# Kernel optimization log

Measured on AMD Instinct MI355X. Metric: run time of the kernel, lower is better.

## Reference

```python
import jax, jax.numpy as jnp
import numpy as np

B, S, HID = 2, 2048, 1024
H, KV, D = 16, 8, 64
NDIM = 2          # position_ids.shape[-1]
EPS = 1e-6
SCALING = 1.0


def _rms_norm(x, w=None, eps=EPS):
    # matches _RMSNorm: fp32 compute, optional learnable scale
    xf = x.astype(jnp.float32)
    n = xf * jax.lax.rsqrt(jnp.mean(xf * xf, axis=-1, keepdims=True) + eps)
    if w is not None:
        n = n * w.astype(jnp.float32)
    return n.astype(x.dtype)


def _rotate_half(x):
    d = x.shape[-1] // 2
    return jnp.concatenate([-x[..., d:], x[..., :d]], axis=-1)


def _apply_multidim_rope(x, cos, sin, ndim):
    # x: [B,S,h,D]; cos/sin: [B,S,D]; unsqueeze_dim=2 broadcasts over heads
    num_channels = x.shape[-1]
    cpd = 2 * (num_channels // (2 * ndim))  # channels per RoPE dimension
    outs = []
    for k in range(ndim):
        sl = slice(k * cpd, (k + 1) * cpd)
        xk = x[..., sl]
        ck = cos[..., sl][:, :, None, :]
        sk = sin[..., sl][:, :, None, :]
        outs.append(xk * ck + _rotate_half(xk) * sk)
    return jnp.concatenate(outs, axis=-1)


def setup_inputs() -> dict:
    key = jax.random.key(0)
    ks = jax.random.split(key, 10)
    scale = 0.02
    return {
        "hidden_states": jax.random.normal(ks[0], (B, S, HID), jnp.float32),
        "cos": jax.random.normal(ks[1], (B, S, D), jnp.float32),
        "sin": jax.random.normal(ks[2], (B, S, D), jnp.float32),
        "position_ids": jax.random.randint(ks[3], (B, S, NDIM), 0, 64, jnp.int64),
        "Wq": jax.random.normal(ks[4], (HID, H * D), jnp.float32) * scale,
        "Wk": jax.random.normal(ks[5], (HID, KV * D), jnp.float32) * scale,
        "Wv": jax.random.normal(ks[6], (HID, KV * D), jnp.float32) * scale,
        "Wo": jax.random.normal(ks[7], (H * D, HID), jnp.float32) * scale,
        "q_norm_w": jnp.ones((D,), jnp.float32),
        "k_norm_w": jnp.ones((D,), jnp.float32),
    }


def reference(hidden_states, cos, sin, position_ids, Wq, Wk, Wv, Wo, q_norm_w, k_norm_w):
    ndim = position_ids.shape[-1]
    bsz, seq_len, _ = hidden_states.shape

    q = (hidden_states @ Wq).reshape(bsz, seq_len, H, D)
    q = _rms_norm(q, q_norm_w)
    q = _apply_multidim_rope(q, cos, sin, ndim)
    q = jnp.transpose(q, (0, 2, 1, 3))  # [B,H,S,D]

    k = (hidden_states @ Wk).reshape(bsz, seq_len, KV, D)
    k = _rms_norm(k, k_norm_w)
    k = _apply_multidim_rope(k, cos, sin, ndim)
    k = jnp.transpose(k, (0, 2, 1, 3))  # [B,KV,S,D]

    v = (hidden_states @ Wv).reshape(bsz, seq_len, KV, D)
    v = _rms_norm(v, None)  # v_norm has no scale
    v = jnp.transpose(v, (0, 2, 1, 3))  # [B,KV,S,D]

    groups = H // KV
    if groups > 1:
        k = jnp.repeat(k, groups, axis=1)  # [B,H,S,D]
        v = jnp.repeat(v, groups, axis=1)

    scores = jnp.einsum("bhqd,bhkd->bhqk", q, k) * SCALING
    attn = jax.nn.softmax(scores.astype(jnp.float32), axis=-1).astype(q.dtype)
    out = jnp.einsum("bhqk,bhkd->bhqd", attn, v)
    out = jnp.transpose(out, (0, 2, 1, 3)).reshape(bsz, seq_len, H * D)
    return out @ Wo
```

## Files before the change

kernel.cpp:

```cpp
#include <hip/hip_runtime.h>

#define PB 2
#define PS 2048
#define PHID 1024
#define PH 16
#define PKV 8
#define PD 64
#define PM (PB*PS)
#define PR (PB*PH*PS)

typedef _Float16 f16_t;
typedef _Float16 f16x8 __attribute__((ext_vector_type(8)));
typedef _Float16 f16x2 __attribute__((ext_vector_type(2)));
typedef float f32x4 __attribute__((ext_vector_type(4)));

#define MFMAH(a,b,c)  __builtin_amdgcn_mfma_f32_16x16x32_f16((a),(b),(c),0,0,0)
#define LOG2E 1.44269504f

__device__ __forceinline__ void gl16(const f16_t* g, f16_t* l) {
  __builtin_amdgcn_global_load_lds(
      (const __attribute__((address_space(1))) void*)g,
      (__attribute__((address_space(3))) void*)l, 16, 0, 0);
}

__global__ __launch_bounds__(256)
void convert_hs(const float* __restrict__ hs, f16_t* __restrict__ hf)
{
  const size_t i = ((size_t)blockIdx.x * 256 + threadIdx.x) * 8;
  float4 a = *(const float4*)&hs[i];
  float4 b = *(const float4*)&hs[i + 4];
  float xs[8] = {a.x, a.y, a.z, a.w, b.x, b.y, b.z, b.w};
  f16x8 v;
  #pragma unroll
  for (int j = 0; j < 8; ++j) v[j] = (f16_t)xs[j];
  *(f16x8*)&hf[i] = v;
}

__global__ __launch_bounds__(256)
void convert_w(const float* __restrict__ Wq, const float* __restrict__ Wk,
               const float* __restrict__ Wv, const float* __restrict__ Wo,
               f16_t* __restrict__ wtT)
{
  __shared__ float Tt[64][68];
  const int tid = threadIdx.x;
  const int slot = blockIdx.x >> 4, k0 = (blockIdx.x & 15) * 64;

  const float* src; int N, ncol0, orow0;
  if (slot < 16)      { src = Wq; N = 1024; ncol0 = slot*64;      orow0 = slot*64; }
  else if (slot < 24) { src = Wk; N = 512;  ncol0 = (slot-16)*64; orow0 = 1024 + (slot-16)*64; }
  else if (slot < 32) { src = Wv; N = 512;  ncol0 = (slot-24)*64; orow0 = 1536 + (slot-24)*64; }
  else                { src = Wo; N = 1024; ncol0 = (slot-32)*64; orow0 = 2048 + (slot-32)*64; }

  const int tk = tid >> 6, tn = tid & 63;
  #pragma unroll
  for (int i = 0; i < 16; ++i)
    Tt[tn][tk*16 + i] = src[(size_t)(k0 + tk*16 + i) * N + ncol0 + tn];
  __syncthreads();

  const int n = tid >> 2, kc = (tid & 3) * 16;
  f16x8 a0, a1;
  #pragma unroll
  for (int i = 0; i < 8; ++i) {
    a0[i] = (f16_t)Tt[n][kc + i];
    a1[i] = (f16_t)Tt[n][kc + 8 + i];
  }
  const size_t ob = (size_t)(orow0 + n) * 1024 + k0 + kc;
  *(f16x8*)&wtT[ob]     = a0;
  *(f16x8*)&wtT[ob + 8] = a1;
}

__global__ __launch_bounds__(256)
void qkv_kernel(const f16_t* __restrict__ hsf, const f16_t* __restrict__ wtT,
                const float* __restrict__ cosp, const float* __restrict__ sinp,
                const float* __restrict__ qnw, const float* __restrict__ knw,
                f16_t* __restrict__ q_o, f16_t* __restrict__ k_o,
                f16_t* __restrict__ vt_o)
{
  __shared__ __align__(16) f16_t Ah[128][64];
  __shared__ __align__(16) f16_t Bh[64][64];

  const int tid = threadIdx.x;
  const int lane = tid & 63, wave = tid >> 6;
  const int lo16 = lane & 15, hi4 = lane >> 4;
  const int lin = blockIdx.x;
  const int swz = (lin & 7) * 128 + (lin >> 3);
  const int m0 = (swz >> 5) * 128;
  const int slot = swz & 31;

  int kind, hd, orow;
  if (slot < 16)      { kind = 0; hd = slot;      orow = slot*64; }
  else if (slot < 24) { kind = 1; hd = slot - 16; orow = 1024 + hd*64; }
  else                { kind = 2; hd = slot - 24; orow = 1536 + hd*64; }

  f32x4 acc[2][4];
  #pragma unroll
  for (int qb = 0; qb < 2; ++qb)
    #pragma unroll
    for (int j = 0; j < 4; ++j) acc[qb][j] = f32x4{0.f, 0.f, 0.f, 0.f};

  const int ri = lane >> 3, pc = lane & 7;
  const int lcs = (pc ^ ri) * 8;
  size_t aoff4[4]; f16_t* aldst4[4];
  #pragma unroll
  for (int q = 0; q < 4; ++q) {
    aoff4[q] = (size_t)(m0 + wave*32 + q*8 + ri) * PHID + lcs;
    aldst4[q] = &Ah[wave*32 + q*8][0];
  }
  size_t boff[2]; int brow[2];
  #pragma unroll
  for (int q = 0; q < 2; ++q) {
    brow[q] = wave*16 + q*8;
    boff[q] = (size_t)(orow + brow[q] + ri) * 1024 + lcs;
  }

  const int rsw = lo16 & 7;

  for (int k0 = 0; k0 < PHID; k0 += 64) {
    __syncthreads();
    #pragma unroll
    for (int q = 0; q < 4; ++q) gl16(hsf + aoff4[q] + k0, aldst4[q]);
    #pragma unroll
    for (int q = 0; q < 2; ++q) gl16(wtT + boff[q] + k0, &Bh[brow[q]][0]);
    __syncthreads();

    #pragma unroll
    for (int t = 0; t < 2; ++t) {
      const int ccol = ((t*4 + hi4) ^ rsw) * 8;
      f16x8 ah[2];
      #pragma unroll
      for (int qb = 0; qb < 2; ++qb)
        ah[qb] = *(const f16x8*)&Ah[wave*32 + qb*16 + lo16][ccol];
      #pragma unroll
      for (int j = 0; j < 4; ++j) {
        f16x8 bh = *(const f16x8*)&Bh[j*16 + lo16][ccol];
        #pragma unroll
        for (int qb = 0; qb < 2; ++qb)
          acc[qb][j] = MFMAH(ah[qb], bh, acc[qb][j]);
      }
    }
  }

  #pragma unroll
  for (int qb = 0; qb < 2; ++qb) {
    float scale[4];
    #pragma unroll
    for (int r = 0; r < 4; ++r) {
      float s = 0.f;
      #pragma unroll
      for (int j = 0; j < 4; ++j) s += acc[qb][j][r] * acc[qb][j][r];
      #pragma unroll
      for (int m = 1; m < 16; m <<= 1) s += __shfl_xor(s, m);
      scale[r] = 1.0f / sqrtf(s * (1.0f/64.0f) + 1e-6f);
    }
    float nw[4];
    #pragma unroll
    for (int j = 0; j < 4; ++j)
      nw[j] = (kind == 0) ? qnw[lo16 + 16*j] : (kind == 1 ? knw[lo16 + 16*j] : 1.0f);

    float y[4][4];
    #pragma unroll
    for (int j = 0; j < 4; ++j)
      #pragma unroll
      for (int r = 0; r < 4; ++r) y[j][r] = acc[qb][j][r] * scale[r] * nw[j];

    if (kind == 2) {
      #pragma unroll
      for (int r = 0; r < 4; ++r) {
        int mg = m0 + wave*32 + qb*16 + hi4*4 + r;
        int b = mg >> 11, sq = mg & 2047;
        int g = sq & 63;
        int sp = (g & 3) | (((g >> 4) & 1) << 2) | (((g >> 2) & 1) << 3)
               | (((g >> 3) & 1) << 4) | (g & 32);
        int sq2 = (sq & ~63) | sp;
        #pragma unroll
        for (int j = 0; j < 4; ++j) {
          int d = lo16 + 16*j;
          vt_o[((size_t)((b*PKV + hd)*PD + d))*PS + sq2] = (f16_t)y[j][r];
        }
      }
    } else {
      #pragma unroll
      for (int r = 0; r < 4; ++r) {
        int mg = m0 + wave*32 + qb*16 + hi4*4 + r;
        int b = mg >> 11, sq = mg & 2047;
        const float* cp = &cosp[(size_t)mg * PD];
        const float* sp = &sinp[(size_t)mg * PD];
        float z[4];
        #pragma unroll
        for (int j = 0; j < 4; ++j) {
          float c = cp[lo16 + 16*j], s = sp[lo16 + 16*j];
          float rot = (j & 1) ? y[j-1][r] : -y[j+1][r];
          z[j] = y[j][r] * c + rot * s;
        }
        #pragma unroll
        for (int j = 0; j < 4; ++j) {
          int d = lo16 + 16*j;
          if (kind == 0) {
            size_t idx = ((size_t)(b*PH + hd)*PS + sq)*PD + d;
            q_o[idx] = (f16_t)(z[j] * LOG2E);
          } else {
            size_t idx = ((size_t)(b*PKV + hd)*PS + sq)*PD + d;
            k_o[idx] = (f16_t)z[j];
          }
        }
      }
    }
  }
}

__global__ __launch_bounds__(256, 4)
void attn_kernel(const f16_t* __restrict__ q_g, const f16_t* __restrict__ k_g,
                 const f16_t* __restrict__ vt_g,
                 f16_t* __restrict__ op, float2* __restrict__ ml)
{
  __shared__ __align__(16) char lds_raw[32768];
  f16_t (*Ks)[64][64] = (f16_t (*)[64][64])lds_raw;
  f16_t (*Vs)[64][64] = (f16_t (*)[64][64])(lds_raw + 16384);
  f16_t (*Ob)[72]     = (f16_t (*)[72])lds_raw;

  const int tid = threadIdx.x, lane = tid & 63, wave = tid >> 6;
  const int lo16 = lane & 15, hi4 = lane >> 4;
  const int lin = blockIdx.x;
  const int swz = (lin & 7) * 128 + (lin >> 3);
  const int qt = swz & 15;
  const int bh = (swz >> 4) & 31;
  const int ks = swz >> 9;
  const int b = bh >> 4, h = bh & 15, kvh = h >> 1;

  f16x8 qf[2][2];
  #pragma unroll
  for (int qb = 0; qb < 2; ++qb) {
    const size_t qbase = ((size_t)(b*PH + h)*PS + qt*128 + wave*32 + qb*16 + lo16) * PD;
    #pragma unroll
    for (int t = 0; t < 2; ++t)
      qf[qb][t] = *(const f16x8*)&q_g[qbase + t*32 + hi4*8];
  }

  f32x4 o[2][4];
  float mq[2] = {-1e30f, -1e30f}, lq[2] = {0.f, 0.f};
  #pragma unroll
  for (int qb = 0; qb < 2; ++qb)
    #pragma unroll
    for (int j = 0; j < 4; ++j) o[qb][j] = f32x4{0.f, 0.f, 0.f, 0.f};

  const int ri = lane >> 3;
  const int lcs = ((lane & 7) ^ ri) * 8;
  const size_t kbase = (size_t)(b*PKV + kvh) * PS * PD + (size_t)ks * 1024 * PD;
  const size_t vbase = (size_t)(b*PKV + kvh) * PD * PS + (size_t)ks * 1024;

  auto STAGE = [&](int kt, int buf) {
    const f16_t* kp = k_g + kbase + (size_t)kt * 64 * PD;
    const f16_t* vp = vt_g + vbase + kt * 64;
    #pragma unroll
    for (int i = 0; i < 2; ++i) {
      const int st = wave*2 + i;
      gl16(kp + (st*8 + ri)*PD + lcs, &Ks[buf][st*8][0]);
      gl16(vp + (size_t)(st*8 + ri)*PS + lcs, &Vs[buf][st*8][0]);
    }
  };

  STAGE(0, 0);
  int cur = 0;
  const int rsw = lo16 & 7;

  for (int kt = 0; kt < 16; ++kt) {
    __syncthreads();
    if (kt + 1 < 16) STAGE(kt + 1, cur ^ 1);

    f32x4 sacc[2][4];
    #pragma unroll
    for (int qb = 0; qb < 2; ++qb)
      #pragma unroll
      for (int j = 0; j < 4; ++j) sacc[qb][j] = f32x4{0.f, 0.f, 0.f, 0.f};
    __builtin_amdgcn_s_setprio(1);
    #pragma unroll
    for (int j = 0; j < 4; ++j) {
      #pragma unroll
      for (int t = 0; t < 2; ++t) {
        f16x8 kf = *(const f16x8*)&Ks[cur][j*16 + lo16][((t*4 + hi4) ^ rsw) * 8];
        #pragma unroll
        for (int qb = 0; qb < 2; ++qb)
          sacc[qb][j] = MFMAH(kf, qf[qb][t], sacc[qb][j]);
      }
    }
    __builtin_amdgcn_s_setprio(0);

    #pragma unroll
    for (int qb = 0; qb < 2; ++qb) {
      float tm = sacc[qb][0][0];
      #pragma unroll
      for (int j = 0; j < 4; ++j)
        #pragma unroll
        for (int r = 0; r < 4; ++r) tm = fmaxf(tm, sacc[qb][j][r]);
      tm = fmaxf(tm, __shfl_xor(tm, 16));
      tm = fmaxf(tm, __shfl_xor(tm, 32));
      if (!__all(tm <= mq[qb] + 8.0f)) {
        float mnew = fmaxf(mq[qb], tm);
        float alpha = __builtin_amdgcn_exp2f(mq[qb] - mnew);
        lq[qb] *= alpha;
        #pragma unroll
        for (int jd = 0; jd < 4; ++jd) o[qb][jd] *= alpha;
        mq[qb] = mnew;
      }
      float ls = 0.f;
      #pragma unroll
      for (int j = 0; j < 4; ++j)
        #pragma unroll
        for (int r = 0; r < 4; ++r) {
          float p = __builtin_amdgcn_exp2f(sacc[qb][j][r] - mq[qb]);
          sacc[qb][j][r] = p;
          ls += p;
        }
      ls += __shfl_xor(ls, 16);
      ls += __shfl_xor(ls, 32);
      lq[qb] += ls;
    }

    f16x8 pa[2][2];
    #pragma unroll
    for (int qb = 0; qb < 2; ++qb)
      #pragma unroll
      for (int t = 0; t < 2; ++t) {
        f16x8 v;
        #pragma unroll
        for (int e = 0; e < 8; ++e)
          v[e] = (f16_t)sacc[qb][2*t + (e >> 2)][e & 3];
        pa[qb][t] = v;
      }

    __builtin_amdgcn_s_setprio(1);
    #pragma unroll
    for (int jd = 0; jd < 4; ++jd) {
      #pragma unroll
      for (int t = 0; t < 2; ++t) {
        f16x8 vf = *(const f16x8*)&Vs[cur][jd*16 + lo16][((t*4 + hi4) ^ rsw) * 8];
        #pragma unroll
        for (int qb = 0; qb < 2; ++qb)
          o[qb][jd] = MFMAH(vf, pa[qb][t], o[qb][jd]);
      }
    }
    __builtin_amdgcn_s_setprio(0);

    cur ^= 1;
  }

  __syncthreads();
  const int rbase = bh*PS + qt*128 + wave*32;
  if (hi4 == 0) {
    #pragma unroll
    for (int qb = 0; qb < 2; ++qb)
      ml[(size_t)ks*PR + rbase + qb*16 + lo16] = float2{mq[qb], lq[qb]};
  }
  #pragma unroll
  for (int qb = 0; qb < 2; ++qb) {
    float inv = 1.0f / lq[qb];
    #pragma unroll
    for (int jd = 0; jd < 4; ++jd)
      #pragma unroll
      for (int rp = 0; rp < 2; ++rp)
        *(f16x2*)&Ob[wave*32 + qb*16 + lo16][jd*16 + hi4*4 + 2*rp] =
            f16x2{(f16_t)(o[qb][jd][2*rp] * inv), (f16_t)(o[qb][jd][2*rp+1] * inv)};
  }
  {
    const int row = lane >> 1, half = lane & 1;
    const size_t gb_ = ((size_t)ks*PR + rbase + row) * PD + half*32;
    #pragma unroll
    for (int c = 0; c < 4; ++c)
      *(f16x8*)&op[gb_ + c*8] = *(const f16x8*)&Ob[wave*32 + row][half*32 + c*8];
  }
}

__global__ __launch_bounds__(256)
void merge_kernel(const f16_t* __restrict__ op, const float2* __restrict__ ml,
                  f16_t* __restrict__ ao)
{
  const int gid = blockIdx.x * 256 + threadIdx.x;
  const int row = gid >> 3, oct = gid & 7;
  float2 e0 = ml[row], e1 = ml[PR + row];
  float M = fmaxf(e0.x, e1.x);
  float c0 = __builtin_amdgcn_exp2f(e0.x - M) * e0.y;
  float c1 = __builtin_amdgcn_exp2f(e1.x - M) * e1.y;
  float inv = 1.0f / (c0 + c1);
  c0 *= inv; c1 *= inv;
  f16x8 a = *(const f16x8*)&op[(size_t)row*PD + oct*8];
  f16x8 bq = *(const f16x8*)&op[(size_t)(PR + row)*PD + oct*8];
  f16x8 r;
  #pragma unroll
  for (int i = 0; i < 8; ++i)
    r[i] = (f16_t)(c0 * (float)a[i] + c1 * (float)bq[i]);
  const int bh = row >> 11, sq = row & 2047;
  const int b = bh >> 4, h = bh & 15;
  *(f16x8*)&ao[((size_t)(b*PS + sq))*PHID + h*PD + oct*8] = r;
}

__global__ __launch_bounds__(256)
void oproj_kernel(const f16_t* __restrict__ ao, const f16_t* __restrict__ woT,
                  float* __restrict__ out)
{
  __shared__ __align__(16) f16_t As[128][40], Bs[64][40];
  const int tid = threadIdx.x;
  const int lane = tid & 63, wave = tid >> 6;
  const int lo16 = lane & 15, hi4 = lane >> 4;
  const int lin = blockIdx.x;
  const int swz = (lin & 7) * 64 + (lin >> 3);
  const int m0 = (swz >> 4) * 128;
  const int col0 = (swz & 15) * 64;

  f32x4 acc[2][4];
  #pragma unroll
  for (int qb = 0; qb < 2; ++qb)
    #pragma unroll
    for (int j = 0; j < 4; ++j) acc[qb][j] = f32x4{0.f, 0.f, 0.f, 0.f};

  const int ar = tid >> 1, akc = (tid & 1) * 16;
  const int bn = tid & 63, bkc = (tid >> 6) * 8;

  f16x8 gA0, gA1, gB;
  auto LOADA = [&](int k0) {
    const f16_t* ap = &ao[(size_t)(m0 + ar) * PHID + k0 + akc];
    gA0 = *(const f16x8*)ap;
    gA1 = *(const f16x8*)(ap + 8);
  };
  auto LOADB = [&](int k0) {
    gB = *(const f16x8*)&woT[(size_t)(col0 + bn) * 1024 + k0 + bkc];
  };
  LOADA(0); LOADB(0);

  for (int k0 = 0; k0 < PHID; k0 += 32) {
    __syncthreads();
    *(f16x8*)&As[ar][akc]     = gA0;
    *(f16x8*)&As[ar][akc + 8] = gA1;
    *(f16x8*)&Bs[bn][bkc]     = gB;
    if (k0 + 32 < PHID) { LOADA(k0 + 32); LOADB(k0 + 32); }
    __syncthreads();
    {
      f16x8 a[2];
      #pragma unroll
      for (int qb = 0; qb < 2; ++qb)
        a[qb] = *(const f16x8*)&As[wave*32 + qb*16 + lo16][hi4*8];
      #pragma unroll
      for (int j = 0; j < 4; ++j) {
        f16x8 bb = *(const f16x8*)&Bs[j*16 + lo16][hi4*8];
        #pragma unroll
        for (int qb = 0; qb < 2; ++qb)
          acc[qb][j] = MFMAH(a[qb], bb, acc[qb][j]);
      }
    }
  }

  #pragma unroll
  for (int qb = 0; qb < 2; ++qb)
    #pragma unroll
    for (int r = 0; r < 4; ++r) {
      int mg = m0 + wave*32 + qb*16 + hi4*4 + r;
      #pragma unroll
      for (int j = 0; j < 4; ++j)
        out[(size_t)mg*PHID + col0 + lo16 + 16*j] = acc[qb][j][r];
    }
}

extern "C" void kernel_launch(void* const* d_in, const int* in_sizes, int n_in,
                              void* d_out, int out_size, void* d_ws, size_t ws_size,
                              hipStream_t stream) {
  (void)in_sizes; (void)n_in; (void)out_size; (void)ws_size;
  const float* hs   = (const float*)d_in[0];
  const float* cosp = (const float*)d_in[1];
  const float* sinp = (const float*)d_in[2];
  const float* Wq   = (const float*)d_in[4];
  const float* Wk   = (const float*)d_in[5];
  const float* Wv   = (const float*)d_in[6];
  const float* Wo   = (const float*)d_in[7];
  const float* qnw  = (const float*)d_in[8];
  const float* knw  = (const float*)d_in[9];
  float* out = (float*)d_out;

  const size_t QN = (size_t)PB*PH*PS*PD;
  const size_t KN = (size_t)PB*PKV*PS*PD;
  const size_t HN = (size_t)PM*PHID;
  char* wsb = (char*)d_ws;
  f16_t*  qv  = (f16_t*)wsb;
  f16_t*  kv  = qv + QN;
  f16_t*  vt  = kv + KN;
  f16_t*  hsf = vt + KN;
  f16_t*  wtT = hsf + HN;
  f16_t*  op  = wtT + (size_t)3072*1024;
  float2* ml  = (float2*)(op + 2*QN);
  f16_t*  ao  = qv;
  const f16_t* woT = wtT + (size_t)2048*1024;

  convert_hs<<<dim3(2048), 256, 0, stream>>>(hs, hsf);
  convert_w <<<dim3(768),  256, 0, stream>>>(Wq, Wk, Wv, Wo, wtT);
  qkv_kernel<<<dim3(1024), 256, 0, stream>>>(hsf, wtT, cosp, sinp,
                                             qnw, knw, qv, kv, vt);
  attn_kernel<<<dim3(1024), 256, 0, stream>>>(qv, kv, vt, op, ml);
  merge_kernel<<<dim3(PR*8/256), 256, 0, stream>>>(op, ml, ao);
  oproj_kernel<<<dim3(512), 256, 0, stream>>>(ao, woT, out);
}
```

Measured before the change: 126.6 us.

## Widen QKV GEMM tile to two heads per block and streamline attention softmax

The QKV projection kernel now computes a 128x128 output tile (two heads) per block instead of 128x64. This halves the grid and reuses each staged hidden-state tile across twice as many MFMAs, cutting redundant A-tile loads, at the cost of more accumulator registers and a larger LDS footprint. The attention kernel also drops the explicit zeroing of the score accumulators by chaining the MFMA from a zero constant. It fuses the exp2 computation with the f16 packing of P and uses a tree-shaped max reduction, aiming to trim VALU work and register pressure.

Result: faster. 119.2 us (-5.9%).

```diff
diff --git a/kernel.cpp b/kernel.cpp
--- a/kernel.cpp
+++ b/kernel.cpp
@@ -77,40 +77,38 @@
                 f16_t* __restrict__ vt_o)
 {
   __shared__ __align__(16) f16_t Ah[128][64];
-  __shared__ __align__(16) f16_t Bh[64][64];
+  __shared__ __align__(16) f16_t Bh[128][64];
 
   const int tid = threadIdx.x;
   const int lane = tid & 63, wave = tid >> 6;
   const int lo16 = lane & 15, hi4 = lane >> 4;
   const int lin = blockIdx.x;
-  const int swz = (lin & 7) * 128 + (lin >> 3);
-  const int m0 = (swz >> 5) * 128;
-  const int slot = swz & 31;
-
-  int kind, hd, orow;
-  if (slot < 16)      { kind = 0; hd = slot;      orow = slot*64; }
-  else if (slot < 24) { kind = 1; hd = slot - 16; orow = 1024 + hd*64; }
-  else                { kind = 2; hd = slot - 24; orow = 1536 + hd*64; }
-
-  f32x4 acc[2][4];
+  const int swz = (lin & 7) * 64 + (lin >> 3);
+  const int m0 = (swz >> 4) * 128;
+  const int ws = swz & 15;
+  const int orow = ws * 128;
+
+  int kind, hd0;
+  if (ws < 8)       { kind = 0; hd0 = ws*2; }
+  else if (ws < 12) { kind = 1; hd0 = (ws-8)*2; }
+  else              { kind = 2; hd0 = (ws-12)*2; }
+
+  f32x4 acc[2][8];
   #pragma unroll
   for (int qb = 0; qb < 2; ++qb)
     #pragma unroll
-    for (int j = 0; j < 4; ++j) acc[qb][j] = f32x4{0.f, 0.f, 0.f, 0.f};
+    for (int j = 0; j < 8; ++j) acc[qb][j] = f32x4{0.f, 0.f, 0.f, 0.f};
 
   const int ri = lane >> 3, pc = lane & 7;
   const int lcs = (pc ^ ri) * 8;
   size_t aoff4[4]; f16_t* aldst4[4];
+  size_t boff4[4]; f16_t* bldst4[4];
   #pragma unroll
   for (int q = 0; q < 4; ++q) {
     aoff4[q] = (size_t)(m0 + wave*32 + q*8 + ri) * PHID + lcs;
     aldst4[q] = &Ah[wave*32 + q*8][0];
-  }
-  size_t boff[2]; int brow[2];
-  #pragma unroll
-  for (int q = 0; q < 2; ++q) {
-    brow[q] = wave*16 + q*8;
-    boff[q] = (size_t)(orow + brow[q] + ri) * 1024 + lcs;
+    boff4[q] = (size_t)(orow + wave*32 + q*8 + ri) * 1024 + lcs;
+    bldst4[q] = &Bh[wave*32 + q*8][0];
   }
 
   const int rsw = lo16 & 7;
@@ -120,7 +118,7 @@
     #pragma unroll
     for (int q = 0; q < 4; ++q) gl16(hsf + aoff4[q] + k0, aldst4[q]);
     #pragma unroll
-    for (int q = 0; q < 2; ++q) gl16(wtT + boff[q] + k0, &Bh[brow[q]][0]);
+    for (int q = 0; q < 4; ++q) gl16(wtT + boff4[q] + k0, bldst4[q]);
     __syncthreads();
 
     #pragma unroll
@@ -131,7 +129,7 @@
       for (int qb = 0; qb < 2; ++qb)
         ah[qb] = *(const f16x8*)&Ah[wave*32 + qb*16 + lo16][ccol];
       #pragma unroll
-      for (int j = 0; j < 4; ++j) {
+      for (int j = 0; j < 8; ++j) {
         f16x8 bh = *(const f16x8*)&Bh[j*16 + lo16][ccol];
         #pragma unroll
         for (int qb = 0; qb < 2; ++qb)
@@ -140,28 +138,38 @@
     }
   }
 
+  float nwv[4];
+  #pragma unroll
+  for (int jj = 0; jj < 4; ++jj)
+    nwv[jj] = (kind == 0) ? qnw[lo16 + 16*jj]
+            : (kind == 1) ? knw[lo16 + 16*jj] : 1.0f;
+
   #pragma unroll
   for (int qb = 0; qb < 2; ++qb) {
-    float scale[4];
+    float sc[2][4];
     #pragma unroll
     for (int r = 0; r < 4; ++r) {
-      float s = 0.f;
-      #pragma unroll
-      for (int j = 0; j < 4; ++j) s += acc[qb][j][r] * acc[qb][j][r];
-      #pragma unroll
-      for (int m = 1; m < 16; m <<= 1) s += __shfl_xor(s, m);
-      scale[r] = 1.0f / sqrtf(s * (1.0f/64.0f) + 1e-6f);
-    }
-    float nw[4];
-    #pragma unroll
-    for (int j = 0; j < 4; ++j)
-      nw[j] = (kind == 0) ? qnw[lo16 + 16*j] : (kind == 1 ? knw[lo16 + 16*j] : 1.0f);
-
-    float y[4][4];
-    #pragma unroll
-    for (int j = 0; j < 4; ++j)
-      #pragma unroll
-      for (int r = 0; r < 4; ++r) y[j][r] = acc[qb][j][r] * scale[r] * nw[j];
+      float s0 = 0.f, s1 = 0.f;
+      #pragma unroll
+      for (int j = 0; j < 4; ++j) {
+        s0 += acc[qb][j][r]   * acc[qb][j][r];
+        s1 += acc[qb][j+4][r] * acc[qb][j+4][r];
+      }
+      #pragma unroll
+      for (int m = 1; m < 16; m <<= 1) {
+        s0 += __shfl_xor(s0, m);
+        s1 += __shfl_xor(s1, m);
+      }
+      sc[0][r] = 1.0f / sqrtf(s0 * (1.0f/64.0f) + 1e-6f);
+      sc[1][r] = 1.0f / sqrtf(s1 * (1.0f/64.0f) + 1e-6f);
+    }
+
+    float y[8][4];
+    #pragma unroll
+    for (int j = 0; j < 8; ++j)
+      #pragma unroll
+      for (int r = 0; r < 4; ++r)
+        y[j][r] = acc[qb][j][r] * sc[j>>2][r] * nwv[j&3];
 
     if (kind == 2) {
       #pragma unroll
@@ -173,8 +181,8 @@
                | (((g >> 3) & 1) << 4) | (g & 32);
         int sq2 = (sq & ~63) | sp;
         #pragma unroll
-        for (int j = 0; j < 4; ++j) {
-          int d = lo16 + 16*j;
+        for (int j = 0; j < 8; ++j) {
+          int d = lo16 + 16*(j & 3), hd = hd0 + (j >> 2);
           vt_o[((size_t)((b*PKV + hd)*PD + d))*PS + sq2] = (f16_t)y[j][r];
         }
       }
@@ -185,16 +193,17 @@
         int b = mg >> 11, sq = mg & 2047;
         const float* cp = &cosp[(size_t)mg * PD];
         const float* sp = &sinp[(size_t)mg * PD];
-        float z[4];
-        #pragma unroll
-        for (int j = 0; j < 4; ++j) {
-          float c = cp[lo16 + 16*j], s = sp[lo16 + 16*j];
+        float z[8];
+        #pragma unroll
+        for (int j = 0; j < 8; ++j) {
+          int d = lo16 + 16*(j & 3);
+          float c = cp[d], s = sp[d];
           float rot = (j & 1) ? y[j-1][r] : -y[j+1][r];
           z[j] = y[j][r] * c + rot * s;
         }
         #pragma unroll
-        for (int j = 0; j < 4; ++j) {
-          int d = lo16 + 16*j;
+        for (int j = 0; j < 8; ++j) {
+          int d = lo16 + 16*(j & 3), hd = hd0 + (j >> 2);
           if (kind == 0) {
             size_t idx = ((size_t)(b*PH + hd)*PS + sq)*PD + d;
             q_o[idx] = (f16_t)(z[j] * LOG2E);
@@ -243,6 +252,8 @@
     #pragma unroll
     for (int j = 0; j < 4; ++j) o[qb][j] = f32x4{0.f, 0.f, 0.f, 0.f};
 
+  const f32x4 FZ = {0.f, 0.f, 0.f, 0.f};
+
   const int ri = lane >> 3;
   const int lcs = ((lane & 7) ^ ri) * 8;
   const size_t kbase = (size_t)(b*PKV + kvh) * PS * PD + (size_t)ks * 1024 * PD;
@@ -268,30 +279,29 @@
     if (kt + 1 < 16) STAGE(kt + 1, cur ^ 1);
 
     f32x4 sacc[2][4];
-    #pragma unroll
-    for (int qb = 0; qb < 2; ++qb)
-      #pragma unroll
-      for (int j = 0; j < 4; ++j) sacc[qb][j] = f32x4{0.f, 0.f, 0.f, 0.f};
     __builtin_amdgcn_s_setprio(1);
     #pragma unroll
     for (int j = 0; j < 4; ++j) {
-      #pragma unroll
-      for (int t = 0; t < 2; ++t) {
-        f16x8 kf = *(const f16x8*)&Ks[cur][j*16 + lo16][((t*4 + hi4) ^ rsw) * 8];
-        #pragma unroll
-        for (int qb = 0; qb < 2; ++qb)
-          sacc[qb][j] = MFMAH(kf, qf[qb][t], sacc[qb][j]);
-      }
+      f16x8 kf0 = *(const f16x8*)&Ks[cur][j*16 + lo16][(hi4 ^ rsw) * 8];
+      f16x8 kf1 = *(const f16x8*)&Ks[cur][j*16 + lo16][((4 + hi4) ^ rsw) * 8];
+      #pragma unroll
+      for (int qb = 0; qb < 2; ++qb)
+        sacc[qb][j] = MFMAH(kf1, qf[qb][1], MFMAH(kf0, qf[qb][0], FZ));
     }
     __builtin_amdgcn_s_setprio(0);
 
+    f16x8 pa[2][2];
     #pragma unroll
     for (int qb = 0; qb < 2; ++qb) {
-      float tm = sacc[qb][0][0];
-      #pragma unroll
-      for (int j = 0; j < 4; ++j)
-        #pragma unroll
-        for (int r = 0; r < 4; ++r) tm = fmaxf(tm, sacc[qb][j][r]);
+      float x0 = fmaxf(fmaxf(sacc[qb][0][0], sacc[qb][0][1]),
+                       fmaxf(sacc[qb][0][2], sacc[qb][0][3]));
+      float x1 = fmaxf(fmaxf(sacc[qb][1][0], sacc[qb][1][1]),
+                       fmaxf(sacc[qb][1][2], sacc[qb][1][3]));
+      float x2 = fmaxf(fmaxf(sacc[qb][2][0], sacc[qb][2][1]),
+                       fmaxf(sacc[qb][2][2], sacc[qb][2][3]));
+      float x3 = fmaxf(fmaxf(sacc[qb][3][0], sacc[qb][3][1]),
+                       fmaxf(sacc[qb][3][2], sacc[qb][3][3]));
+      float tm = fmaxf(fmaxf(x0, x1), fmaxf(x2, x3));
       tm = fmaxf(tm, __shfl_xor(tm, 16));
       tm = fmaxf(tm, __shfl_xor(tm, 32));
       if (!__all(tm <= mq[qb] + 8.0f)) {
@@ -304,29 +314,20 @@
       }
       float ls = 0.f;
       #pragma unroll
-      for (int j = 0; j < 4; ++j)
-        #pragma unroll
-        for (int r = 0; r < 4; ++r) {
-          float p = __builtin_amdgcn_exp2f(sacc[qb][j][r] - mq[qb]);
-          sacc[qb][j][r] = p;
+      for (int t = 0; t < 2; ++t) {
+        f16x8 v;
+        #pragma unroll
+        for (int e = 0; e < 8; ++e) {
+          float p = __builtin_amdgcn_exp2f(sacc[qb][2*t + (e >> 2)][e & 3] - mq[qb]);
           ls += p;
+          v[e] = (f16_t)p;
         }
+        pa[qb][t] = v;
+      }
       ls += __shfl_xor(ls, 16);
       ls += __shfl_xor(ls, 32);
       lq[qb] += ls;
     }
-
-    f16x8 pa[2][2];
-    #pragma unroll
-    for (int qb = 0; qb < 2; ++qb)
-      #pragma unroll
-      for (int t = 0; t < 2; ++t) {
-        f16x8 v;
-        #pragma unroll
-        for (int e = 0; e < 8; ++e)
-          v[e] = (f16_t)sacc[qb][2*t + (e >> 2)][e & 3];
-        pa[qb][t] = v;
-      }
 
     __builtin_amdgcn_s_setprio(1);
     #pragma unroll
@@ -490,7 +491,7 @@
 
   convert_hs<<<dim3(2048), 256, 0, stream>>>(hs, hsf);
   convert_w <<<dim3(768),  256, 0, stream>>>(Wq, Wk, Wv, Wo, wtT);
-  qkv_kernel<<<dim3(1024), 256, 0, stream>>>(hsf, wtT, cosp, sinp,
+  qkv_kernel<<<dim3(512),  256, 0, stream>>>(hsf, wtT, cosp, sinp,
                                              qnw, knw, qv, kv, vt);
   attn_kernel<<<dim3(1024), 256, 0, stream>>>(qv, kv, vt, op, ml);
   merge_kernel<<<dim3(PR*8/256), 256, 0, stream>>>(op, ml, ao);
```
